# Optimization experiments

Measured on AMD Instinct MI355X. Metric: run time of the kernel, lower is better.

Reference implementation:

```python
import jax, jax.numpy as jnp
import numpy as np

EPS = 1e-5

def _linear(x, w, b):
    # torch nn.Linear convention: w is [out, in]
    return jnp.einsum('...i,oi->...o', x, w) + b

def _l2_normalize(x, axis=-1):
    n = jnp.sqrt(jnp.sum(x * x, axis=axis, keepdims=True))
    return x / jnp.maximum(n, 1e-12)

def _online_softmax_scan(sim):
    # sim: [B, H, L]. Running max m_t and running sum s_t = sum_{i<=t} exp(sim_i - m_t)
    def combine(a, b):
        ma, sa = a
        mb, sb = b
        m = jnp.maximum(ma, mb)
        s = sa * jnp.exp(ma - m) + sb * jnp.exp(mb - m)
        return m, s
    m_scan, s_scan = jax.lax.associative_scan(combine, (sim, jnp.ones_like(sim)), axis=2)
    return m_scan, s_scan


def setup_inputs() -> dict:
    key = jax.random.key(0)
    ks = jax.random.split(key, 8)
    B, L, D = 2, 2048, 256
    H, h = 8, 32
    s = 1.0 / np.sqrt(D)
    inp = {
        'x': jax.random.normal(ks[0], (B, L, D), jnp.float32),
        'wq_w': jax.random.normal(ks[1], (D, D), jnp.float32) * s,
        'wq_b': jnp.zeros((D,), jnp.float32),
        'wk_w': jax.random.normal(ks[2], (D, D), jnp.float32) * s,
        'wk_b': jnp.zeros((D,), jnp.float32),
        'wv_w': jax.random.normal(ks[3], (D, D), jnp.float32) * s,
        'wv_b': jnp.zeros((D,), jnp.float32),
        'wo_w': jax.random.normal(ks[4], (D, D), jnp.float32) * s,
        'wo_b': jnp.zeros((D,), jnp.float32),
        'wg_w': jax.random.normal(ks[5], (1, h * h), jnp.float32) * (1.0 / np.sqrt(h * h)),
        'wg_b': jnp.zeros((1,), jnp.float32),
        'kv_norm_scale': jnp.ones((1, H, 1, h, h), jnp.float32),
        'qk_norm_scale': jnp.full((1, H, 1), 1.0 / np.sqrt(h), jnp.float32),
    }
    return inp


def reference(x, wq_w, wq_b, wk_w, wk_b, wv_w, wv_b, wo_w, wo_b,
              wg_w, wg_b, kv_norm_scale, qk_norm_scale):
    B, L, D = x.shape
    H, h = kv_norm_scale.shape[1], kv_norm_scale.shape[3]

    q = _linear(x, wq_w, wq_b).reshape(B, L, H, h).transpose(0, 2, 1, 3)  # bhld
    k = _linear(x, wk_w, wk_b).reshape(B, L, H, h).transpose(0, 2, 1, 3)
    v = _linear(x, wv_w, wv_b).reshape(B, L, H, h).transpose(0, 2, 1, 3)

    sim = jnp.einsum('bhld,bhld->bhl', q, k) * qk_norm_scale  # [B,H,L]

    k = _l2_normalize(k)
    v = _l2_normalize(v)

    # outer-product KV state per position: [B,H,L,h,h]
    Z = jnp.einsum('bhld,bhle->bhlde', v, k) * kv_norm_scale

    # gating: squared ReLU of linear over flattened h*h features
    gate_inputs = Z.reshape(B, H, L, h * h)
    gates_logits = jnp.einsum('bhli,oi->bhlo', gate_inputs, wg_w) + wg_b  # [B,H,L,1]
    gates = jnp.square(jax.nn.relu(gates_logits)) + EPS
    gates = gates[..., None]  # [B,H,L,1,1]
    gated_Z = gates * Z

    # associative scans along L
    m_scan, s_scan = _online_softmax_scan(sim)        # [B,H,L]
    Z_scan = jnp.cumsum(gated_Z, axis=2)              # [B,H,L,h,h]
    g_scan = jnp.cumsum(gates, axis=2)                # [B,H,L,1,1]

    softmax_weights = (jnp.exp(sim - m_scan) / (s_scan + EPS))[..., None, None]
    gated_weights = Z_scan / (g_scan + EPS)
    attn_weights = gated_weights * (1.0 + jax.nn.silu(softmax_weights))

    ctxt = jnp.einsum('bhld,bhlde->bhle', q, attn_weights)
    ctxt = ctxt.transpose(0, 2, 1, 3).reshape(B, L, D)
    return _linear(ctxt, wo_w, wo_b)
```

## Files before the change

### kernel.cpp

```cpp
#include <hip/hip_runtime.h>
#include <math.h>

#define EPSV 1e-5f

static constexpr int Ls = 2048, Hh = 8;
static constexpr int NCH = 64, T = 32;

typedef unsigned short u16;
using frag  = __attribute__((ext_vector_type(8))) short;
using f32x4 = __attribute__((ext_vector_type(4))) float;

__device__ __forceinline__ void split_bf16(float v, u16& hi, u16& lo) {
    const unsigned u = __float_as_uint(v);
    hi = (u16)(u >> 16);
    const float hf = __uint_as_float((unsigned)hi << 16);
    lo = (u16)(__float_as_uint(v - hf) >> 16);
}

__device__ __forceinline__ unsigned pk2(u16 a, u16 b) {
    return (unsigned)a | ((unsigned)b << 16);
}

__device__ __forceinline__ void split8(const float4& a, const float4& b,
                                       uint4& hi, uint4& lo) {
    u16 h[8], l[8];
    const float f[8] = {a.x, a.y, a.z, a.w, b.x, b.y, b.z, b.w};
#pragma unroll
    for (int i = 0; i < 8; ++i) split_bf16(f[i], h[i], l[i]);
    hi = make_uint4(pk2(h[0], h[1]), pk2(h[2], h[3]), pk2(h[4], h[5]), pk2(h[6], h[7]));
    lo = make_uint4(pk2(l[0], l[1]), pk2(l[2], l[3]), pk2(l[4], l[5]), pk2(l[6], l[7]));
}

__global__ __launch_bounds__(256) void qkv_fused(
    const float* __restrict__ x,
    const float* __restrict__ wq, const float* __restrict__ wk, const float* __restrict__ wv,
    const float* __restrict__ bq, const float* __restrict__ bk, const float* __restrict__ bv,
    const float* __restrict__ wg_w, const float* __restrict__ wg_b,
    const float* __restrict__ kvs, const float* __restrict__ qks,
    float* __restrict__ qh, float* __restrict__ kh, float* __restrict__ vh,
    float* __restrict__ simG, float* __restrict__ gG,
    float* __restrict__ ZcT, float* __restrict__ mT, float* __restrict__ sT,
    float* __restrict__ gTt,
    float* __restrict__ aW, float* __restrict__ bW, int* __restrict__ flagW)
{
    constexpr int LDK = 40;
    constexpr int LDT = 68;
    __shared__ __align__(16) float smemf[3 * 64 * LDT];
    __shared__ __align__(16) float wkT[2 * 1152];
    __shared__ float lsim[128], lg2[128];

    u16* As_hi = (u16*)smemf;
    u16* As_lo = As_hi + 2560;
    u16* Wst   = As_lo + 2560;
    float* Qt = smemf;
    float* Kt = Qt + 64 * LDT;
    float* Vt = Kt + 64 * LDT;

    const int tid = threadIdx.x;
    const int mt = blockIdx.x, nt = blockIdx.y;
    const int m0 = mt * 64, ncol0 = nt * 64;
    const int bidx = m0 >> 11, lg = m0 & (Ls - 1);
    const int wave = tid >> 6, lane = tid & 63;
    const int l15 = lane & 15, quad = lane >> 4;
    const int srow = tid >> 2, sk = (tid & 3) * 8;

    for (int i = tid; i < 2048; i += 256) {
        const int h = i >> 10, de = i & 1023;
        const int d = de >> 5, e = de & 31;
        wkT[h * 1152 + e * 36 + d] = wg_w[de] * kvs[(nt * 2 + h) * 1024 + de];
    }

    const float* Wsrc[3] = {wq, wk, wv};
    f32x4 acc[3][4] = {};

    float4 a0 = *(const float4*)&x[(size_t)(m0 + srow) * 256 + sk];
    float4 a1 = *(const float4*)&x[(size_t)(m0 + srow) * 256 + sk + 4];
    float4 w0[3], w1[3];
#pragma unroll
    for (int w = 0; w < 3; ++w) {
        w0[w] = *(const float4*)&Wsrc[w][(size_t)(ncol0 + srow) * 256 + sk];
        w1[w] = *(const float4*)&Wsrc[w][(size_t)(ncol0 + srow) * 256 + sk + 4];
    }

    for (int it = 0; it < 8; ++it) {
        __syncthreads();
        {
            uint4 hi, lo;
            split8(a0, a1, hi, lo);
            *(uint4*)&As_hi[srow * LDK + sk] = hi;
            *(uint4*)&As_lo[srow * LDK + sk] = lo;
#pragma unroll
            for (int w = 0; w < 3; ++w) {
                split8(w0[w], w1[w], hi, lo);
                *(uint4*)&Wst[w * 5120 + srow * LDK + sk] = hi;
                *(uint4*)&Wst[w * 5120 + 2560 + srow * LDK + sk] = lo;
            }
        }
        __syncthreads();

        if (it < 7) {
            const int k0 = (it + 1) * 32;
            a0 = *(const float4*)&x[(size_t)(m0 + srow) * 256 + k0 + sk];
            a1 = *(const float4*)&x[(size_t)(m0 + srow) * 256 + k0 + sk + 4];
#pragma unroll
            for (int w = 0; w < 3; ++w) {
                w0[w] = *(const float4*)&Wsrc[w][(size_t)(ncol0 + srow) * 256 + k0 + sk];
                w1[w] = *(const float4*)&Wsrc[w][(size_t)(ncol0 + srow) * 256 + k0 + sk + 4];
            }
        }

        frag ah[4], al[4];
#pragma unroll
        for (int tm = 0; tm < 4; ++tm) {
            const int r = tm * 16 + l15;
            ah[tm] = *(const frag*)&As_hi[r * LDK + quad * 8];
            al[tm] = *(const frag*)&As_lo[r * LDK + quad * 8];
        }
#pragma unroll
        for (int w = 0; w < 3; ++w) {
            const u16* bp = &Wst[w * 5120 + (wave * 16 + l15) * LDK + quad * 8];
            const frag bh = *(const frag*)bp;
            const frag bl = *(const frag*)(bp + 2560);
#pragma unroll
            for (int tm = 0; tm < 4; ++tm) {
                acc[w][tm] = __builtin_amdgcn_mfma_f32_16x16x32_bf16(ah[tm], bh, acc[w][tm], 0, 0, 0);
                acc[w][tm] = __builtin_amdgcn_mfma_f32_16x16x32_bf16(ah[tm], bl, acc[w][tm], 0, 0, 0);
                acc[w][tm] = __builtin_amdgcn_mfma_f32_16x16x32_bf16(al[tm], bh, acc[w][tm], 0, 0, 0);
            }
        }
    }
    __syncthreads();

    {
        float* tiles[3] = {Qt, Kt, Vt};
        const float* biases[3] = {bq, bk, bv};
#pragma unroll
        for (int w = 0; w < 3; ++w) {
            const int col = wave * 16 + l15;
            const float bias = biases[w][ncol0 + col];
#pragma unroll
            for (int tm = 0; tm < 4; ++tm)
#pragma unroll
                for (int r = 0; r < 4; ++r) {
                    const int m = tm * 16 + quad * 4 + r;
                    tiles[w][m * LDT + col] = acc[w][tm][r] + bias;
                }
        }
    }
    __syncthreads();

    if (tid < 128) {
        const int h = tid >> 6, l = tid & 63;
        const int rb = l * LDT + h * 32;
        float4 kr[8], vr[8];
        float ksum = 0.f, vsum = 0.f, qk = 0.f;
#pragma unroll
        for (int e4 = 0; e4 < 8; ++e4) {
            kr[e4] = *(const float4*)&Kt[rb + e4 * 4];
            vr[e4] = *(const float4*)&Vt[rb + e4 * 4];
            const float4 q4 = *(const float4*)&Qt[rb + e4 * 4];
            ksum += kr[e4].x * kr[e4].x + kr[e4].y * kr[e4].y + kr[e4].z * kr[e4].z + kr[e4].w * kr[e4].w;
            vsum += vr[e4].x * vr[e4].x + vr[e4].y * vr[e4].y + vr[e4].z * vr[e4].z + vr[e4].w * vr[e4].w;
            qk   += q4.x * kr[e4].x + q4.y * kr[e4].y + q4.z * kr[e4].z + q4.w * kr[e4].w;
        }
        const float kscale = 1.f / fmaxf(sqrtf(ksum), 1e-12f);
        const float vscale = 1.f / fmaxf(sqrtf(vsum), 1e-12f);
#pragma unroll
        for (int e4 = 0; e4 < 8; ++e4) {
            float4 k4 = kr[e4], v4 = vr[e4];
            k4.x *= kscale; k4.y *= kscale; k4.z *= kscale; k4.w *= kscale;
            v4.x *= vscale; v4.y *= vscale; v4.z *= vscale; v4.w *= vscale;
            *(float4*)&Kt[rb + e4 * 4] = k4;
            *(float4*)&Vt[rb + e4 * 4] = v4;
        }
        const float sim = qk * qks[nt * 2 + h];
        lsim[h * 64 + l] = sim;
        simG[(size_t)(bidx * 8 + nt * 2 + h) * Ls + lg + l] = sim;
    }
    __syncthreads();

    {
        const float* tl[3] = {Qt, Kt, Vt};
        float* gl[3] = {qh, kh, vh};
#pragma unroll
        for (int arr = 0; arr < 3; ++arr)
#pragma unroll
            for (int it = 0; it < 4; ++it) {
                const int idx = it * 1024 + tid * 4;
                const int h = idx >> 11, rem = idx & 2047;
                const int l = rem >> 5, e4 = rem & 31;
                const float4 v = *(const float4*)&tl[arr][l * LDT + h * 32 + e4];
                *(float4*)&gl[arr][(size_t)(bidx * 8 + nt * 2 + h) * 65536 +
                                   (size_t)(lg + l) * 32 + e4] = v;
            }
    }

    {
        const int task = tid >> 1, half = tid & 1;
        const int h = task >> 6, l = task & 63;
        float4 vr[8];
#pragma unroll
        for (int d4 = 0; d4 < 8; ++d4)
            vr[d4] = *(const float4*)&Vt[l * LDT + h * 32 + d4 * 4];
        float u = 0.f;
        const int e0 = half * 16;
#pragma unroll 4
        for (int e = e0; e < e0 + 16; ++e) {
            float4 s4 = make_float4(0.f, 0.f, 0.f, 0.f);
#pragma unroll
            for (int d4 = 0; d4 < 8; ++d4) {
                const float4 w4 = *(const float4*)&wkT[h * 1152 + e * 36 + d4 * 4];
                s4.x = fmaf(vr[d4].x, w4.x, s4.x);
                s4.y = fmaf(vr[d4].y, w4.y, s4.y);
                s4.z = fmaf(vr[d4].z, w4.z, s4.z);
                s4.w = fmaf(vr[d4].w, w4.w, s4.w);
            }
            u = fmaf(s4.x + s4.y + s4.z + s4.w, Kt[l * LDT + h * 32 + e], u);
        }
        u += __shfl_xor(u, 1);
        if (half == 0) {
            const float r = fmaxf(u + wg_b[0], 0.f);
            const float g = r * r + EPSV;
            lg2[h * 64 + l] = g;
            gG[(size_t)(bidx * 8 + nt * 2 + h) * Ls + lg + l] = g;
        }
    }
    __syncthreads();

    {
        const int d = tid >> 3, e4m = (tid & 7) * 4;
#pragma unroll
        for (int h = 0; h < 2; ++h)
#pragma unroll
            for (int cc = 0; cc < 2; ++cc) {
                float4 z4 = make_float4(0.f, 0.f, 0.f, 0.f);
#pragma unroll 8
                for (int l = 0; l < 32; ++l) {
                    const int lr = cc * 32 + l;
                    const float gv = lg2[h * 64 + lr] * Vt[lr * LDT + h * 32 + d];
                    const float4 k4 = *(const float4*)&Kt[lr * LDT + h * 32 + e4m];
                    z4.x = fmaf(gv, k4.x, z4.x);
                    z4.y = fmaf(gv, k4.y, z4.y);
                    z4.z = fmaf(gv, k4.z, z4.z);
                    z4.w = fmaf(gv, k4.w, z4.w);
                }
                const int bhg = bidx * 8 + nt * 2 + h;
                const int cg = (lg >> 5) + cc;
                *(float4*)&ZcT[((size_t)bhg * NCH + cg) * 1024 + d * 32 + e4m] = z4;
            }
    }

    {
        const int h = wave >> 1, cc = wave & 1;
        if (lane < 32) {
            const int lr = cc * 32 + lane;
            float m = lsim[h * 64 + lr], s = 1.f, g = lg2[h * 64 + lr];
#pragma unroll
            for (int off = 16; off; off >>= 1) {
                const float mo = __shfl_xor(m, off);
                const float so = __shfl_xor(s, off);
                const float mn = fmaxf(m, mo);
                s = s * __expf(m - mn) + so * __expf(mo - mn);
                m = mn;
                g += __shfl_xor(g, off);
            }
            if (lane == 0) {
                const int bhg = bidx * 8 + nt * 2 + h;
                const int cg = (lg >> 5) + cc;
                mT[bhg * NCH + cg] = m;
                sT[bhg * NCH + cg] = s;
                gTt[bhg * NCH + cg] = g;
            }
        }
    }

    if (mt == 0 && nt == 0) {
        const int h = tid >> 5, e = tid & 31;
        const float* K = kvs + h * 1024;
        const float k00 = K[0];
        int ok = (k00 != 0.0f);
        for (int d = 0; d < 32; ++d) {
            const float lhs = K[d * 32 + e] * k00;
            const float rhs = K[d * 32] * K[e];
            const float diff = fabsf(lhs - rhs);
            if (diff > 1e-6f * fmaxf(fmaxf(fabsf(lhs), fabsf(rhs)), 1e-20f)) ok = 0;
        }
        aW[h * 32 + e] = K[e * 32];
        bW[h * 32 + e] = (k00 != 0.0f) ? K[e] / k00 : 0.f;
        const int allok = __syncthreads_and(ok);
        if (tid == 0) flagW[0] = allok;
    }
}

__global__ __launch_bounds__(256) void chunk_out_kernel(
    const float* __restrict__ qh, const float* __restrict__ knG, const float* __restrict__ vnG,
    const float* __restrict__ simG, const float* __restrict__ gG,
    const float* __restrict__ kvs,
    const float* __restrict__ ZcT, const float* __restrict__ mT,
    const float* __restrict__ sT, const float* __restrict__ gTt,
    const float* __restrict__ aW, const float* __restrict__ bW,
    const int* __restrict__ flagW,
    u16* __restrict__ chi, u16* __restrict__ clo)
{
    __shared__ __align__(16) float qa[1024], knb[1024], zp[1024], sW[1024];
    __shared__ __align__(16) float vnT[32 * 36];
    __shared__ float lkvs[1024];
    __shared__ float lgS[32], lsimS[32], lwgt[32];
    const int tid = threadIdx.x;
    const int c = blockIdx.x, bh = blockIdx.y, h = bh & 7, b = bh >> 3;
    const int l = tid >> 3, e4 = (tid & 7) * 4;
    const size_t base4 = ((size_t)bh * Ls + (size_t)c * T) * 8 + tid;
    const int flag = flagW[0];

    {
        const float4* Zt = (const float4*)ZcT + (size_t)bh * NCH * 256 + tid;
        float4 zacc = make_float4(0.f, 0.f, 0.f, 0.f);
        int cb = 0;
        for (; cb + 8 <= c; cb += 8) {
            float4 v[8];
#pragma unroll
            for (int i = 0; i < 8; ++i) v[i] = Zt[(size_t)(cb + i) * 256];
#pragma unroll
            for (int i = 0; i < 8; ++i) {
                zacc.x += v[i].x; zacc.y += v[i].y; zacc.z += v[i].z; zacc.w += v[i].w;
            }
        }
        for (; cb < c; ++cb) {
            const float4 v = Zt[(size_t)cb * 256];
            zacc.x += v.x; zacc.y += v.y; zacc.z += v.z; zacc.w += v.w;
        }
        *(float4*)&zp[tid * 4] = zacc;
    }

    const float4 qv4 = ((const float4*)qh)[base4];
    const float4 kn4 = ((const float4*)knG)[base4];
    const float4 vn4 = ((const float4*)vnG)[base4];
    const float4 la4 = *(const float4*)&aW[h * 32 + e4];
    const float4 lb4 = *(const float4*)&bW[h * 32 + e4];
    if (tid < 32) {
        lgS[tid] = gG[bh * Ls + c * T + tid];
        lsimS[tid] = simG[bh * Ls + c * T + tid];
    }
    if (!flag) {
        *(float4*)&lkvs[tid * 4] = *(const float4*)&kvs[h * 1024 + tid * 4];
    }
    {
        float4 q = qv4, k = kn4;
        if (flag) {
            q.x *= la4.x; q.y *= la4.y; q.z *= la4.z; q.w *= la4.w;
            k.x *= lb4.x; k.y *= lb4.y; k.z *= lb4.z; k.w *= lb4.w;
        }
        *(float4*)&qa[l * 32 + e4] = q;
        *(float4*)&knb[l * 32 + e4] = k;
        vnT[(e4 + 0) * 36 + l] = vn4.x;
        vnT[(e4 + 1) * 36 + l] = vn4.y;
        vnT[(e4 + 2) * 36 + l] = vn4.z;
        vnT[(e4 + 3) * 36 + l] = vn4.w;
    }
    __syncthreads();

    if (tid < 64) {
        float mC = mT[bh * NCH + tid], sC = sT[bh * NCH + tid], gC = gTt[bh * NCH + tid];
#pragma unroll
        for (int off = 1; off < 64; off <<= 1) {
            const float mo = __shfl_up(mC, off);
            const float so = __shfl_up(sC, off);
            const float go = __shfl_up(gC, off);
            if (tid >= off) {
                const float mn = fmaxf(mC, mo);
                sC = sC * __expf(mC - mn) + so * __expf(mo - mn);
                mC = mn;
                gC += go;
            }
        }
        const float mp = (c > 0) ? __shfl(mC, c - 1) : -1e30f;
        const float sp = (c > 0) ? __shfl(sC, c - 1) : 0.f;
        const float gp = (c > 0) ? __shfl(gC, c - 1) : 0.f;

        if (tid < 32) {
            float m = lsimS[tid], s = 1.f, g = lgS[tid];
#pragma unroll
            for (int off = 1; off < 32; off <<= 1) {
                const float mo = __shfl_up(m, off);
                const float so = __shfl_up(s, off);
                const float go = __shfl_up(g, off);
                if (tid >= off) {
                    const float mn = fmaxf(m, mo);
                    s = s * __expf(m - mn) + so * __expf(mo - mn);
                    m = mn;
                    g += go;
                }
            }
            const float mn = fmaxf(mp, m);
            s = sp * __expf(mp - mn) + s * __expf(m - mn);
            m = mn;
            g += gp;
            const float sw = __expf(lsimS[tid] - m) / (s + EPSV);
            const float sig = 1.f / (1.f + __expf(-sw));
            lwgt[tid] = (1.f + sw * sig) / (g + EPSV);
        }
    }

    float4 y4 = make_float4(0.f, 0.f, 0.f, 0.f);
    if (flag) {
        float qrow[32];
#pragma unroll
        for (int d4 = 0; d4 < 8; ++d4)
            *(float4*)&qrow[d4 * 4] = *(const float4*)&qa[l * 32 + d4 * 4];
        float4 s4 = make_float4(0.f, 0.f, 0.f, 0.f);
#pragma unroll 8
        for (int d = 0; d < 32; ++d) {
            const float qd = qrow[d];
            const float4 v4 = *(const float4*)&vnT[d * 36 + e4];
            const float4 p4 = *(const float4*)&zp[d * 32 + e4];
            s4.x = fmaf(qd, v4.x, s4.x);
            s4.y = fmaf(qd, v4.y, s4.y);
            s4.z = fmaf(qd, v4.z, s4.z);
            s4.w = fmaf(qd, v4.w, s4.w);
            y4.x = fmaf(qd, p4.x, y4.x);
            y4.y = fmaf(qd, p4.y, y4.y);
            y4.z = fmaf(qd, p4.z, y4.z);
            y4.w = fmaf(qd, p4.w, y4.w);
        }
        y4.x *= lb4.x; y4.y *= lb4.y; y4.z *= lb4.z; y4.w *= lb4.w;
        const float4 lg4 = *(const float4*)&lgS[e4];
        float4 sm;
        sm.x = (e4 + 0 <= l) ? lg4.x * s4.x : 0.f;
        sm.y = (e4 + 1 <= l) ? lg4.y * s4.y : 0.f;
        sm.z = (e4 + 2 <= l) ? lg4.z * s4.z : 0.f;
        sm.w = (e4 + 3 <= l) ? lg4.w * s4.w : 0.f;
        *(float4*)&sW[l * 32 + e4] = sm;
        __syncthreads();
        float srow[32];
#pragma unroll
        for (int j4 = 0; j4 < 8; ++j4)
            *(float4*)&srow[j4 * 4] = *(const float4*)&sW[l * 32 + j4 * 4];
#pragma unroll 8
        for (int j = 0; j < 32; ++j) {
            const float sj = srow[j];
            const float4 k4 = *(const float4*)&knb[j * 32 + e4];
            y4.x = fmaf(sj, k4.x, y4.x);
            y4.y = fmaf(sj, k4.y, y4.y);
            y4.z = fmaf(sj, k4.z, y4.z);
            y4.w = fmaf(sj, k4.w, y4.w);
        }
    } else {
        __syncthreads();
        float* yp = &y4.x;
#pragma unroll
        for (int ii = 0; ii < 4; ++ii) {
            const int e = e4 + ii;
            float qe[32];
#pragma unroll
            for (int d = 0; d < 32; ++d)
                qe[d] = qa[l * 32 + d] * lkvs[d * 32 + e];
            float y = 0.f;
#pragma unroll
            for (int d = 0; d < 32; ++d)
                y = fmaf(qe[d], zp[d * 32 + e], y);
            for (int j = 0; j < 32; ++j) {
                float s = 0.f;
#pragma unroll
                for (int d = 0; d < 32; ++d)
                    s = fmaf(qe[d], vnT[d * 36 + j], s);
                if (j <= l) y = fmaf(lgS[j] * s, knb[j * 32 + e], y);
            }
            yp[ii] = y;
        }
    }
    const float w = lwgt[l];
    ushort4 hi4, lo4;
    split_bf16(y4.x * w, hi4.x, lo4.x);
    split_bf16(y4.y * w, hi4.y, lo4.y);
    split_bf16(y4.z * w, hi4.z, lo4.z);
    split_bf16(y4.w * w, hi4.w, lo4.w);
    const size_t oidx = ((size_t)(b * Ls + c * T + l)) * 256 + h * 32 + e4;
    *(ushort4*)&chi[oidx] = hi4;
    *(ushort4*)&clo[oidx] = lo4;
}

__global__ __launch_bounds__(256) void out_gemm(
    const u16* __restrict__ Ahi, const u16* __restrict__ Alo,
    const float* __restrict__ wo, const float* __restrict__ bo,
    float* __restrict__ out)
{
    constexpr int LDK = 40;
    __shared__ __align__(16) u16 As_hi[64 * LDK];
    __shared__ __align__(16) u16 As_lo[64 * LDK];
    __shared__ __align__(16) u16 Ws_hi[64 * LDK];
    __shared__ __align__(16) u16 Ws_lo[64 * LDK];

    const int tid = threadIdx.x;
    const int mt = blockIdx.x, nt = blockIdx.y;
    const int m0 = mt * 64, ncol0 = nt * 64;
    const int wave = tid >> 6, lane = tid & 63;
    const int l15 = lane & 15, quad = lane >> 4;
    const int srow = tid >> 2, sk = (tid & 3) * 8;

    f32x4 acc[4] = {};

    uint4 ah = *(const uint4*)&Ahi[(size_t)(m0 + srow) * 256 + sk];
    uint4 al = *(const uint4*)&Alo[(size_t)(m0 + srow) * 256 + sk];
    float4 w0 = *(const float4*)&wo[(size_t)(ncol0 + srow) * 256 + sk];
    float4 w1 = *(const float4*)&wo[(size_t)(ncol0 + srow) * 256 + sk + 4];

    for (int it = 0; it < 8; ++it) {
        __syncthreads();
        {
            uint4 whi, wlo;
            split8(w0, w1, whi, wlo);
            *(uint4*)&As_hi[srow * LDK + sk] = ah;
            *(uint4*)&As_lo[srow * LDK + sk] = al;
            *(uint4*)&Ws_hi[srow * LDK + sk] = whi;
            *(uint4*)&Ws_lo[srow * LDK + sk] = wlo;
        }
        __syncthreads();

        if (it < 7) {
            const int k0 = (it + 1) * 32;
            ah = *(const uint4*)&Ahi[(size_t)(m0 + srow) * 256 + k0 + sk];
            al = *(const uint4*)&Alo[(size_t)(m0 + srow) * 256 + k0 + sk];
            w0 = *(const float4*)&wo[(size_t)(ncol0 + srow) * 256 + k0 + sk];
            w1 = *(const float4*)&wo[(size_t)(ncol0 + srow) * 256 + k0 + sk + 4];
        }

        const frag fah = *(const frag*)&As_hi[(wave * 16 + l15) * LDK + quad * 8];
        const frag fal = *(const frag*)&As_lo[(wave * 16 + l15) * LDK + quad * 8];
#pragma unroll
        for (int cf = 0; cf < 4; ++cf) {
            const frag fbh = *(const frag*)&Ws_hi[(cf * 16 + l15) * LDK + quad * 8];
            const frag fbl = *(const frag*)&Ws_lo[(cf * 16 + l15) * LDK + quad * 8];
            acc[cf] = __builtin_amdgcn_mfma_f32_16x16x32_bf16(fah, fbh, acc[cf], 0, 0, 0);
            acc[cf] = __builtin_amdgcn_mfma_f32_16x16x32_bf16(fah, fbl, acc[cf], 0, 0, 0);
            acc[cf] = __builtin_amdgcn_mfma_f32_16x16x32_bf16(fal, fbh, acc[cf], 0, 0, 0);
        }
    }

#pragma unroll
    for (int cf = 0; cf < 4; ++cf) {
        const int o = ncol0 + cf * 16 + l15;
        const float bias = bo[o];
#pragma unroll
        for (int r = 0; r < 4; ++r) {
            const int rm = m0 + wave * 16 + quad * 4 + r;
            out[(size_t)rm * 256 + o] = acc[cf][r] + bias;
        }
    }
}

extern "C" void kernel_launch(void* const* d_in, const int* in_sizes, int n_in,
                              void* d_out, int out_size, void* d_ws, size_t ws_size,
                              hipStream_t stream) {
    const float* x    = (const float*)d_in[0];
    const float* wq_w = (const float*)d_in[1];
    const float* wq_b = (const float*)d_in[2];
    const float* wk_w = (const float*)d_in[3];
    const float* wk_b = (const float*)d_in[4];
    const float* wv_w = (const float*)d_in[5];
    const float* wv_b = (const float*)d_in[6];
    const float* wo_w = (const float*)d_in[7];
    const float* wo_b = (const float*)d_in[8];
    const float* wg_w = (const float*)d_in[9];
    const float* wg_b = (const float*)d_in[10];
    const float* kvs  = (const float*)d_in[11];
    const float* qks  = (const float*)d_in[12];
    float* out = (float*)d_out;

    u16* chi = (u16*)d_ws;
    u16* clo = chi + 1048576;
    float* qh   = (float*)(clo + 1048576);
    float* kh   = qh + 1048576;
    float* vh   = kh + 1048576;
    float* ZcT  = vh + 1048576;
    float* simG = ZcT + 1048576;
    float* gG   = simG + 32768;
    float* mT   = gG + 32768;
    float* sT   = mT + 1024;
    float* gTt  = sT + 1024;
    float* aW   = gTt + 1024;
    float* bW   = aW + 256;
    int* flagW  = (int*)(bW + 256);

    qkv_fused<<<dim3(64, 4), 256, 0, stream>>>(
        x, wq_w, wk_w, wv_w, wq_b, wk_b, wv_b, wg_w, wg_b, kvs, qks,
        qh, kh, vh, simG, gG, ZcT, mT, sT, gTt, aW, bW, flagW);
    chunk_out_kernel<<<dim3(NCH, 16), 256, 0, stream>>>(
        qh, kh, vh, simG, gG, kvs, ZcT, mT, sT, gTt, aW, bW, flagW, chi, clo);
    out_gemm<<<dim3(64, 4), 256, 0, stream>>>(
        chi, clo, wo_w, wo_b, out);
}
```

Measured before the change: 154.3 us.

## Precompute exclusive prefix of chunk KV states in separate scan kernel

Adds a prefix_kernel that runs a Hillis-Steele exclusive scan over the 64 per-chunk 32x32 KV summaries in shared memory and writes the results back in place. chunk_out_kernel then loads one precomputed prefix tile instead of summing up to 63 earlier chunk tiles per block. This removes quadratic redundant global reads across chunks at the cost of an extra kernel launch and a read-write pass over the chunk buffer.

```diff
diff --git a/kernel.cpp b/kernel.cpp
--- a/kernel.cpp
+++ b/kernel.cpp
@@ -292,11 +292,46 @@
     }
 }
 
+__global__ __launch_bounds__(256) void prefix_kernel(float* __restrict__ Zc)
+{
+    __shared__ float sc[64 * 64];
+    const int bh = blockIdx.x, seg = blockIdx.y;
+    const int tid = threadIdx.x;
+    float* Zb = Zc + (size_t)bh * NCH * 1024 + seg * 64;
+
+#pragma unroll
+    for (int it = 0; it < 16; ++it) {
+        const int idx = it * 256 + tid;
+        const int cc = idx >> 6, e = idx & 63;
+        sc[idx] = Zb[(size_t)cc * 1024 + e];
+    }
+    __syncthreads();
+#pragma unroll
+    for (int st = 1; st < 64; st <<= 1) {
+        float tmp[16];
+#pragma unroll
+        for (int it = 0; it < 16; ++it) {
+            const int idx = it * 256 + tid;
+            tmp[it] = ((idx >> 6) >= st) ? sc[idx - st * 64] : 0.f;
+        }
+        __syncthreads();
+#pragma unroll
+        for (int it = 0; it < 16; ++it) sc[it * 256 + tid] += tmp[it];
+        __syncthreads();
+    }
+#pragma unroll
+    for (int it = 0; it < 16; ++it) {
+        const int idx = it * 256 + tid;
+        const int cc = idx >> 6, e = idx & 63;
+        Zb[(size_t)cc * 1024 + e] = cc ? sc[idx - 64] : 0.f;
+    }
+}
+
 __global__ __launch_bounds__(256) void chunk_out_kernel(
     const float* __restrict__ qh, const float* __restrict__ knG, const float* __restrict__ vnG,
     const float* __restrict__ simG, const float* __restrict__ gG,
     const float* __restrict__ kvs,
-    const float* __restrict__ ZcT, const float* __restrict__ mT,
+    const float* __restrict__ ZcP, const float* __restrict__ mT,
     const float* __restrict__ sT, const float* __restrict__ gTt,
     const float* __restrict__ aW, const float* __restrict__ bW,
     const int* __restrict__ flagW,
@@ -312,29 +347,10 @@
     const size_t base4 = ((size_t)bh * Ls + (size_t)c * T) * 8 + tid;
     const int flag = flagW[0];
 
-    {
-        const float4* Zt = (const float4*)ZcT + (size_t)bh * NCH * 256 + tid;
-        float4 zacc = make_float4(0.f, 0.f, 0.f, 0.f);
-        int cb = 0;
-        for (; cb + 8 <= c; cb += 8) {
-            float4 v[8];
-#pragma unroll
-            for (int i = 0; i < 8; ++i) v[i] = Zt[(size_t)(cb + i) * 256];
-#pragma unroll
-            for (int i = 0; i < 8; ++i) {
-                zacc.x += v[i].x; zacc.y += v[i].y; zacc.z += v[i].z; zacc.w += v[i].w;
-            }
-        }
-        for (; cb < c; ++cb) {
-            const float4 v = Zt[(size_t)cb * 256];
-            zacc.x += v.x; zacc.y += v.y; zacc.z += v.z; zacc.w += v.w;
-        }
-        *(float4*)&zp[tid * 4] = zacc;
-    }
-
     const float4 qv4 = ((const float4*)qh)[base4];
     const float4 kn4 = ((const float4*)knG)[base4];
     const float4 vn4 = ((const float4*)vnG)[base4];
+    const float4 z4  = ((const float4*)ZcP)[((size_t)bh * NCH + c) * 256 + tid];
     const float4 la4 = *(const float4*)&aW[h * 32 + e4];
     const float4 lb4 = *(const float4*)&bW[h * 32 + e4];
     if (tid < 32) {
@@ -352,6 +368,7 @@
         }
         *(float4*)&qa[l * 32 + e4] = q;
         *(float4*)&knb[l * 32 + e4] = k;
+        *(float4*)&zp[tid * 4] = z4;
         vnT[(e4 + 0) * 36 + l] = vn4.x;
         vnT[(e4 + 1) * 36 + l] = vn4.y;
         vnT[(e4 + 2) * 36 + l] = vn4.z;
@@ -584,6 +601,7 @@
     qkv_fused<<<dim3(64, 4), 256, 0, stream>>>(
         x, wq_w, wk_w, wv_w, wq_b, wk_b, wv_b, wg_w, wg_b, kvs, qks,
         qh, kh, vh, simG, gG, ZcT, mT, sT, gTt, aW, bW, flagW);
+    prefix_kernel<<<dim3(16, 16), 256, 0, stream>>>(ZcT);
     chunk_out_kernel<<<dim3(NCH, 16), 256, 0, stream>>>(
         qh, kh, vh, simG, gG, kvs, ZcT, mT, sT, gTt, aW, bW, flagW, chi, clo);
     out_gemm<<<dim3(64, 4), 256, 0, stream>>>(
```

New measurement: 152.8 us. No clear change (-1.0%).
